# Optimization experiments

Hardware: AMD Instinct MI355X
Metric: run time of the kernel (lower is better)

Reference implementation:

```python
import jax, jax.numpy as jnp
import numpy as np

N, F_IN, E = 16384, 512, 524288
H1, H2 = 32, 16


def gcn_conv(x, src, dst, W, b, n):
    # PyG GCNConv: linear (no bias) -> symmetric-normalized neighbor sum
    # (self-loops already appended to src/dst) -> add bias.
    deg = jnp.zeros((n,), x.dtype).at[dst].add(jnp.ones((src.shape[0],), x.dtype))
    dinv = jax.lax.rsqrt(deg)  # deg >= 1 thanks to self-loops
    norm = dinv[src] * dinv[dst]  # [E+N]
    xw = x @ W                    # [N, out]
    msg = xw[src] * norm[:, None] # gather over edges
    out = jnp.zeros((n, W.shape[1]), x.dtype).at[dst].add(msg)  # scatter-add
    return out + b


def setup_inputs() -> dict:
    key = jax.random.key(0)
    ks = jax.random.split(key, 8)
    x = jax.random.normal(ks[0], (N, F_IN), jnp.float32)
    edge_index = jax.random.randint(ks[1], (2, E), 0, N, jnp.int64)
    def glorot(k, shp):
        lim = np.sqrt(6.0 / (shp[0] + shp[1])).astype(np.float32)
        return jax.random.uniform(k, shp, jnp.float32, -lim, lim)
    return {
        "x": x,
        "edge_index": edge_index,
        "W1": glorot(ks[2], (F_IN, H1)), "b1": jnp.zeros((H1,), jnp.float32),
        "W2": glorot(ks[3], (H1, H2)),  "b2": jnp.zeros((H2,), jnp.float32),
        "W3": glorot(ks[4], (H1, H2)),  "b3": jnp.zeros((H2,), jnp.float32),
        "num_nodes": N,
    }


def reference(x, edge_index, W1, b1, W2, b2, W3, b3, num_nodes):
    n = num_nodes
    loops = jnp.arange(n, dtype=edge_index.dtype)
    src = jnp.concatenate([edge_index[0], loops])
    dst = jnp.concatenate([edge_index[1], loops])
    h1 = gcn_conv(x, src, dst, W1, b1, n)
    mu = gcn_conv(h1, src, dst, W2, b2, n)
    logvar = gcn_conv(h1, src, dst, W3, b3, n)
    z = mu  # eval mode: reparameterize returns mu, decoder dropout is a no-op
    adj = jax.nn.sigmoid(z @ z.T)  # [N, N] inner-product decode
    return adj, mu, logvar
```

## Files before the change

### kernel.cpp

```cpp
#include <hip/hip_runtime.h>
#include <hip/hip_bf16.h>

#define N_NODES 16384
#define F_IN    512
#define N_EDGE  524288
#define H1      32
#define H2      16

typedef float f32x4 __attribute__((ext_vector_type(4)));
typedef short bf16x8 __attribute__((ext_vector_type(8)));

#define OFF_CNT     0u
#define OFF_ROWPTR  16448u
#define OFF_CURSOR  32896u
#define OFF_SRCS    49344u
#define OFF_DINV    573632u
#define OFF_XW1     590080u
#define OFF_XW23    1114368u

__device__ __forceinline__ float sigf(float x) {
    float e = __expf(-x);
    return __builtin_amdgcn_rcpf(1.0f + e);
}

__device__ __forceinline__ unsigned short bf16_rne(float f) {
    unsigned u = __float_as_uint(f);
    return (unsigned short)((u + 0x7FFFu + ((u >> 16) & 1u)) >> 16);
}

__global__ __launch_bounds__(256) void hist_k(const int* __restrict__ ei,
                                              unsigned* __restrict__ cnt) {
    int e = blockIdx.x * 256 + threadIdx.x;
    atomicAdd(&cnt[ei[N_EDGE + e]], 1u);
}

__global__ __launch_bounds__(1024) void scan_k(const unsigned* __restrict__ cnt,
                                               unsigned* __restrict__ rowptr,
                                               unsigned* __restrict__ cursor,
                                               float* __restrict__ dinv) {
    const int t = threadIdx.x;
    unsigned vals[16];
    const uint4* c4 = (const uint4*)cnt;
#pragma unroll
    for (int i = 0; i < 4; ++i) {
        uint4 v = c4[t * 4 + i];
        vals[i * 4 + 0] = v.x; vals[i * 4 + 1] = v.y;
        vals[i * 4 + 2] = v.z; vals[i * 4 + 3] = v.w;
    }
    unsigned loc[16], s = 0;
#pragma unroll
    for (int i = 0; i < 16; ++i) { loc[i] = s; s += vals[i]; }

    const int lane = t & 63, w = t >> 6;
    unsigned v = s;
#pragma unroll
    for (int off = 1; off < 64; off <<= 1) {
        unsigned u = __shfl_up(v, off);
        if (lane >= off) v += u;
    }
    __shared__ unsigned wtot[16];
    if (lane == 63) wtot[w] = v;
    __syncthreads();
    if (t == 0) {
        unsigned run = 0;
#pragma unroll
        for (int i = 0; i < 16; ++i) { unsigned x = wtot[i]; wtot[i] = run; run += x; }
        rowptr[N_NODES] = run;
    }
    __syncthreads();
    unsigned base = wtot[w] + v - s;
#pragma unroll
    for (int i = 0; i < 16; ++i) {
        unsigned rp = base + loc[i];
        rowptr[t * 16 + i] = rp;
        cursor[t * 16 + i] = rp;
        dinv[t * 16 + i] = rsqrtf((float)(vals[i] + 1u));
    }
}

__global__ __launch_bounds__(256) void fill_k(const int* __restrict__ ei,
                                              unsigned* __restrict__ cursor,
                                              int* __restrict__ srcs) {
    int e = blockIdx.x * 256 + threadIdx.x;
    int d = ei[N_EDGE + e];
    unsigned p = atomicAdd(&cursor[d], 1u);
    srcs[p] = ei[e];
}

__global__ __launch_bounds__(256) void gemm1_k(const float* __restrict__ x,
                                               const float* __restrict__ W,
                                               float* __restrict__ xw) {
    int tid = blockIdx.x * 256 + threadIdx.x;
    int row = tid >> 3, cq = tid & 7;
    const float4* x4 = (const float4*)(x + (size_t)row * F_IN);
    const float4* W4 = (const float4*)W;
    float ax = 0.f, ay = 0.f, az = 0.f, aw = 0.f;
#pragma unroll 4
    for (int k4 = 0; k4 < F_IN / 4; ++k4) {
        float4 xv = x4[k4];
        float4 w0 = W4[(size_t)(4 * k4 + 0) * 8 + cq];
        float4 w1 = W4[(size_t)(4 * k4 + 1) * 8 + cq];
        float4 w2 = W4[(size_t)(4 * k4 + 2) * 8 + cq];
        float4 w3 = W4[(size_t)(4 * k4 + 3) * 8 + cq];
        ax = fmaf(xv.x, w0.x, ax); ay = fmaf(xv.x, w0.y, ay);
        az = fmaf(xv.x, w0.z, az); aw = fmaf(xv.x, w0.w, aw);
        ax = fmaf(xv.y, w1.x, ax); ay = fmaf(xv.y, w1.y, ay);
        az = fmaf(xv.y, w1.z, az); aw = fmaf(xv.y, w1.w, aw);
        ax = fmaf(xv.z, w2.x, ax); ay = fmaf(xv.z, w2.y, ay);
        az = fmaf(xv.z, w2.z, az); aw = fmaf(xv.z, w2.w, aw);
        ax = fmaf(xv.w, w3.x, ax); ay = fmaf(xv.w, w3.y, ay);
        az = fmaf(xv.w, w3.z, az); aw = fmaf(xv.w, w3.w, aw);
    }
    float4 o; o.x = ax; o.y = ay; o.z = az; o.w = aw;
    ((float4*)xw)[(size_t)row * 8 + cq] = o;
}

__global__ __launch_bounds__(256) void conv1_k(const float* __restrict__ xw1,
                                               const float* __restrict__ dinv,
                                               const int* __restrict__ srcs,
                                               const unsigned* __restrict__ rowptr,
                                               const float* __restrict__ b1,
                                               const float* __restrict__ W2,
                                               const float* __restrict__ W3,
                                               float* __restrict__ xw23) {
    const int t = threadIdx.x;
    const int node = blockIdx.x * 8 + (t >> 5);
    const int c = t & 31;
    unsigned e0 = rowptr[node], e1 = rowptr[node + 1];
    float sum = 0.f;
    for (unsigned e = e0; e < e1; ++e) {
        int s = srcs[e];
        sum = fmaf(xw1[(size_t)s * H1 + c], dinv[s], sum);
    }
    float di = dinv[node];
    float h = fmaf(di, sum, di * di * xw1[(size_t)node * H1 + c]) + b1[c];
    __shared__ float h1s[8][H1 + 1];
    h1s[t >> 5][c] = h;
    __syncthreads();
    const float* Wm = (c < H2) ? W2 : W3;
    int q = c & (H2 - 1);
    float acc = 0.f;
#pragma unroll
    for (int k = 0; k < H1; ++k) acc = fmaf(h1s[t >> 5][k], Wm[k * H2 + q], acc);
    xw23[(size_t)node * 32 + c] = acc;
}

__global__ __launch_bounds__(256) void conv2_k(const float* __restrict__ xw23,
                                               const float* __restrict__ dinv,
                                               const int* __restrict__ srcs,
                                               const unsigned* __restrict__ rowptr,
                                               const float* __restrict__ b2,
                                               const float* __restrict__ b3,
                                               float* __restrict__ out_mu,
                                               float* __restrict__ out_lv,
                                               unsigned short* __restrict__ zhl) {
    const int t = threadIdx.x;
    const int node = blockIdx.x * 8 + (t >> 5);
    const int c = t & 31;
    const int q = c & (H2 - 1);
    unsigned e0 = rowptr[node], e1 = rowptr[node + 1];
    float sum = 0.f;
    for (unsigned e = e0; e < e1; ++e) {
        int s = srcs[e];
        sum = fmaf(xw23[(size_t)s * 32 + c], dinv[s], sum);
    }
    float di = dinv[node];
    float v = fmaf(di, sum, di * di * xw23[(size_t)node * 32 + c]) +
              ((c < H2) ? b2[q] : b3[q]);
    if (c < H2) {
        out_mu[(size_t)node * H2 + q] = v;
        unsigned short hb = bf16_rne(v);
        float hf = __uint_as_float((unsigned)hb << 16);
        unsigned short lb = bf16_rne(v - hf);
        zhl[(size_t)node * 32 + q] = hb;
        zhl[(size_t)node * 32 + 16 + q] = lb;
    } else {
        out_lv[(size_t)node * H2 + q] = v;
    }
}

__global__ __launch_bounds__(256) void adj_k(const unsigned short* __restrict__ zhl,
                                             float* __restrict__ out) {
    __shared__ short zrs[128][40];
    const int t = threadIdx.x;
    const int wave = t >> 6, lane = t & 63;
    const int lrow = lane & 15, g = lane >> 4;
    const int row0 = blockIdx.y << 7, col0 = blockIdx.x << 7;
    const short* zs = (const short*)zhl;

    {
        int r = t >> 1, half = t & 1;
        const uint4* src = (const uint4*)(zs + (size_t)(row0 + r) * 32);
        uint4 a = src[half * 2 + 0];
        uint4 b = src[half * 2 + 1];
        uint4* dst = (uint4*)&zrs[r][half * 16];
        dst[0] = a; dst[1] = b;
    }

    const int cbase = col0 + wave * 32;
    bf16x8 A0 = *(const bf16x8*)(zs + (size_t)(cbase + lrow) * 32 + g * 8);
    bf16x8 A1 = *(const bf16x8*)(zs + (size_t)(cbase + 16 + lrow) * 32 + g * 8);

    __syncthreads();

    f32x4 acc[2][8];
#pragma unroll
    for (int m = 0; m < 2; ++m)
#pragma unroll
        for (int n = 0; n < 8; ++n) acc[m][n] = (f32x4){0.f, 0.f, 0.f, 0.f};

#pragma unroll
    for (int n = 0; n < 8; ++n) {
        const short* rb = &zrs[n * 16 + lrow][0];
        bf16x8 B1 = *(const bf16x8*)(rb + (g & 1) * 8);
        bf16x8 B2 = *(const bf16x8*)(rb + 16 + (g & 1) * 8);
        acc[0][n] = __builtin_amdgcn_mfma_f32_16x16x32_bf16(A0, B1, acc[0][n], 0, 0, 0);
        acc[0][n] = __builtin_amdgcn_mfma_f32_16x16x32_bf16(A0, B2, acc[0][n], 0, 0, 0);
        acc[1][n] = __builtin_amdgcn_mfma_f32_16x16x32_bf16(A1, B1, acc[1][n], 0, 0, 0);
        acc[1][n] = __builtin_amdgcn_mfma_f32_16x16x32_bf16(A1, B2, acc[1][n], 0, 0, 0);
    }

#pragma unroll
    for (int n = 0; n < 8; ++n) {
        size_t rowoff = (size_t)(row0 + n * 16 + lrow) * N_NODES;
#pragma unroll
        for (int m = 0; m < 2; ++m) {
            f32x4 o;
            o.x = sigf(acc[m][n][0]); o.y = sigf(acc[m][n][1]);
            o.z = sigf(acc[m][n][2]); o.w = sigf(acc[m][n][3]);
            *(f32x4*)(out + rowoff + cbase + m * 16 + g * 4) = o;
        }
    }
}

extern "C" void kernel_launch(void* const* d_in, const int* in_sizes, int n_in,
                              void* d_out, int out_size, void* d_ws, size_t ws_size,
                              hipStream_t stream) {
    const float* x  = (const float*)d_in[0];
    const int*   ei = (const int*)d_in[1];
    const float* W1 = (const float*)d_in[2];
    const float* b1 = (const float*)d_in[3];
    const float* W2 = (const float*)d_in[4];
    const float* b2 = (const float*)d_in[5];
    const float* W3 = (const float*)d_in[6];
    const float* b3 = (const float*)d_in[7];
    float* out = (float*)d_out;

    unsigned* ws   = (unsigned*)d_ws;
    unsigned* cnt    = ws + OFF_CNT;
    unsigned* rowptr = ws + OFF_ROWPTR;
    unsigned* cursor = ws + OFF_CURSOR;
    int*      srcs   = (int*)(ws + OFF_SRCS);
    float*    dinv   = (float*)(ws + OFF_DINV);
    float*    xw1    = (float*)(ws + OFF_XW1);
    float*    xw23   = (float*)(ws + OFF_XW23);
    unsigned short* zhl = (unsigned short*)(ws + OFF_XW1);

    float* out_mu = out + (size_t)N_NODES * N_NODES;
    float* out_lv = out_mu + (size_t)N_NODES * H2;

    (void)hipMemsetAsync(cnt, 0, N_NODES * sizeof(unsigned), stream);
    hist_k<<<N_EDGE / 256, 256, 0, stream>>>(ei, cnt);
    scan_k<<<1, 1024, 0, stream>>>(cnt, rowptr, cursor, dinv);
    fill_k<<<N_EDGE / 256, 256, 0, stream>>>(ei, cursor, srcs);
    gemm1_k<<<(N_NODES * 8) / 256, 256, 0, stream>>>(x, W1, xw1);
    conv1_k<<<N_NODES / 8, 256, 0, stream>>>(xw1, dinv, srcs, rowptr, b1, W2, W3, xw23);
    conv2_k<<<N_NODES / 8, 256, 0, stream>>>(xw23, dinv, srcs, rowptr, b2, b3,
                                             out_mu, out_lv, zhl);
    adj_k<<<dim3(N_NODES / 128, N_NODES / 128), 256, 0, stream>>>(zhl, out);
}
```

Baseline: 357.7 us.

## Restructure adj decode into persistent row-strip waves streaming column tiles

The inner-product decode kernel drops its LDS-staged 128x128 tile and barrier. Each wave now holds a 16-row B fragment in registers and loops over 128 consecutive 16-column tiles, loading A directly from global memory and writing sigmoid outputs. The grid shrinks to 2048 blocks so each wave streams long contiguous row segments. The aim is lower launch and synchronization overhead and better write locality, at the cost of fewer independent tiles in flight per wave.

New measurement: 416.1 us. 1.16x slower.

```diff
diff --git a/kernel.cpp b/kernel.cpp
--- a/kernel.cpp
+++ b/kernel.cpp
@@ -181,55 +181,33 @@
 
 __global__ __launch_bounds__(256) void adj_k(const unsigned short* __restrict__ zhl,
                                              float* __restrict__ out) {
-    __shared__ short zrs[128][40];
     const int t = threadIdx.x;
     const int wave = t >> 6, lane = t & 63;
     const int lrow = lane & 15, g = lane >> 4;
-    const int row0 = blockIdx.y << 7, col0 = blockIdx.x << 7;
+    const int strip = blockIdx.x & 511;
+    const int chunk = blockIdx.x >> 9;
     const short* zs = (const short*)zhl;
 
-    {
-        int r = t >> 1, half = t & 1;
-        const uint4* src = (const uint4*)(zs + (size_t)(row0 + r) * 32);
-        uint4 a = src[half * 2 + 0];
-        uint4 b = src[half * 2 + 1];
-        uint4* dst = (uint4*)&zrs[r][half * 16];
-        dst[0] = a; dst[1] = b;
-    }
-
-    const int cbase = col0 + wave * 32;
-    bf16x8 A0 = *(const bf16x8*)(zs + (size_t)(cbase + lrow) * 32 + g * 8);
-    bf16x8 A1 = *(const bf16x8*)(zs + (size_t)(cbase + 16 + lrow) * 32 + g * 8);
-
-    __syncthreads();
-
-    f32x4 acc[2][8];
-#pragma unroll
-    for (int m = 0; m < 2; ++m)
-#pragma unroll
-        for (int n = 0; n < 8; ++n) acc[m][n] = (f32x4){0.f, 0.f, 0.f, 0.f};
-
-#pragma unroll
-    for (int n = 0; n < 8; ++n) {
-        const short* rb = &zrs[n * 16 + lrow][0];
-        bf16x8 B1 = *(const bf16x8*)(rb + (g & 1) * 8);
-        bf16x8 B2 = *(const bf16x8*)(rb + 16 + (g & 1) * 8);
-        acc[0][n] = __builtin_amdgcn_mfma_f32_16x16x32_bf16(A0, B1, acc[0][n], 0, 0, 0);
-        acc[0][n] = __builtin_amdgcn_mfma_f32_16x16x32_bf16(A0, B2, acc[0][n], 0, 0, 0);
-        acc[1][n] = __builtin_amdgcn_mfma_f32_16x16x32_bf16(A1, B1, acc[1][n], 0, 0, 0);
-        acc[1][n] = __builtin_amdgcn_mfma_f32_16x16x32_bf16(A1, B2, acc[1][n], 0, 0, 0);
-    }
-
-#pragma unroll
-    for (int n = 0; n < 8; ++n) {
-        size_t rowoff = (size_t)(row0 + n * 16 + lrow) * N_NODES;
-#pragma unroll
-        for (int m = 0; m < 2; ++m) {
-            f32x4 o;
-            o.x = sigf(acc[m][n][0]); o.y = sigf(acc[m][n][1]);
-            o.z = sigf(acc[m][n][2]); o.w = sigf(acc[m][n][3]);
-            *(f32x4*)(out + rowoff + cbase + m * 16 + g * 4) = o;
-        }
+    const int rbase = (strip << 5) + (wave >> 1) * 16;
+    const int cbase = (chunk << 12) + (wave & 1) * 2048;
+
+    const short* rb = zs + (size_t)(rbase + lrow) * 32;
+    bf16x8 B1 = *(const bf16x8*)(rb + (g & 1) * 8);
+    bf16x8 B2 = *(const bf16x8*)(rb + 16 + (g & 1) * 8);
+
+    size_t rowoff = (size_t)(rbase + lrow) * N_NODES;
+
+#pragma unroll 4
+    for (int n = 0; n < 128; ++n) {
+        int c = cbase + n * 16;
+        bf16x8 A = *(const bf16x8*)(zs + (size_t)(c + lrow) * 32 + g * 8);
+        f32x4 acc = (f32x4){0.f, 0.f, 0.f, 0.f};
+        acc = __builtin_amdgcn_mfma_f32_16x16x32_bf16(A, B1, acc, 0, 0, 0);
+        acc = __builtin_amdgcn_mfma_f32_16x16x32_bf16(A, B2, acc, 0, 0, 0);
+        f32x4 o;
+        o.x = sigf(acc[0]); o.y = sigf(acc[1]);
+        o.z = sigf(acc[2]); o.w = sigf(acc[3]);
+        *(f32x4*)(out + rowoff + c + g * 4) = o;
     }
 }
 
@@ -267,5 +245,5 @@
     conv1_k<<<N_NODES / 8, 256, 0, stream>>>(xw1, dinv, srcs, rowptr, b1, W2, W3, xw23);
     conv2_k<<<N_NODES / 8, 256, 0, stream>>>(xw23, dinv, srcs, rowptr, b2, b3,
                                              out_mu, out_lv, zhl);
-    adj_k<<<dim3(N_NODES / 128, N_NODES / 128), 256, 0, stream>>>(zhl, out);
-}
+    adj_k<<<dim3(2048), 256, 0, stream>>>(zhl, out);
+}
```
